# Optimization experiments

Hardware: AMD Instinct MI355X
Metric: run time of the kernel (lower is better)

Reference implementation:

```python
import jax, jax.numpy as jnp
import numpy as np

B, L, D_IN = 2, 4096, 512
H, D_K, D_V, D_OUT = 8, 64, 64, 512


def setup_inputs() -> dict:
    key = jax.random.key(0)
    k0, k1, k2, k3, k4 = jax.random.split(key, 5)
    x = jax.random.normal(k0, (B, L, D_IN), dtype=jnp.float32)
    W_q = jax.random.uniform(k1, (H, D_IN, D_K), dtype=jnp.float32)
    W_k = jax.random.uniform(k2, (H, D_IN, D_K), dtype=jnp.float32)
    W_v = jax.random.uniform(k3, (H, D_IN, D_V), dtype=jnp.float32)
    W_o = jax.random.uniform(k4, (H, D_V, D_OUT), dtype=jnp.float32)
    return {"x": x, "W_q": W_q, "W_k": W_k, "W_v": W_v, "W_o": W_o}


def reference(x, W_q, W_k, W_v, W_o):
    # x: (b, l, d_in); projections per head -> (b, h, l, d)
    Q = jnp.einsum('hjk,blj->bhlk', W_q, x)
    K = jnp.einsum('hjk,blj->bhlk', W_k, x)
    V = jnp.einsum('hjv,blj->bhlv', W_v, x)
    # no softmax: pure bilinear attention (Q K^T) V
    scores = jnp.einsum('bhik,bhjk->bhij', Q, K)          # (b, h, l, l)
    values = jnp.einsum('bhqk,bhkv->bhqv', scores, V)     # (b, h, l, d_v)
    return jnp.einsum('hvo,bhlv->blo', W_o, values)       # (b, l, d_out)
```

## Files before the change

### kernel.cpp

```cpp
#include <hip/hip_runtime.h>
#include <cstdint>


#define BDIM 2
#define LDIM 4096
#define DIN 512
#define HDIM 8
#define DK 64
#define DV 64
#define DOUT 512
#define NS 16

using bf16_t = __bf16;
typedef __bf16 bf16x8 __attribute__((ext_vector_type(8)));
typedef float floatx4 __attribute__((ext_vector_type(4)));

__device__ __forceinline__ unsigned short f2bf(float f) {
    unsigned int u = __builtin_bit_cast(unsigned int, f);
    u += 0x7FFFu + ((u >> 16) & 1u);
    return (unsigned short)(u >> 16);
}

__device__ __forceinline__ float bf2f(unsigned short s) {
    unsigned int u = ((unsigned int)s) << 16;
    return __builtin_bit_cast(float, u);
}

__device__ __forceinline__ void gld_lds16(const void* g, void* l) {
    __builtin_amdgcn_global_load_lds(
        (const __attribute__((address_space(1))) void*)g,
        (__attribute__((address_space(3))) void*)l, 16, 0, 0);
}

template <int BM, int BN, int BK, bool TRANS_OUT, int OUT_MODE>
__device__ __forceinline__ void gemm_core(const bf16_t* A, const bf16_t* B,
                                          void* Cp, int K, int lda, int ldb,
                                          int ldc, int tm, int tn) {
    constexpr int WM = BM / 2, WN = BN / 2;
    constexpr int FM = WM / 16, FN = WN / 16;
    constexpr int CPR = BK / 8;
    __shared__ bf16_t As[BM * BK];
    __shared__ bf16_t Bs[BN * BK];
    const int tid = threadIdx.x;
    const int lane = tid & 63;
    const int wr = (tid >> 7) & 1;
    const int wc = (tid >> 6) & 1;

    A += (size_t)tm * lda;
    B += (size_t)tn * ldb;

    floatx4 acc[FM][FN] = {};

    for (int k0 = 0; k0 < K; k0 += BK) {
#pragma unroll
        for (int i = 0; i < (BM * CPR) / 256; ++i) {
            int c = i * 256 + tid;
            int m = c / CPR, kc = c % CPR;
            gld_lds16(A + (size_t)m * lda + k0 + kc * 8, As + c * 8);
        }
#pragma unroll
        for (int i = 0; i < (BN * CPR) / 256; ++i) {
            int c = i * 256 + tid;
            int m = c / CPR, kc = c % CPR;
            gld_lds16(B + (size_t)m * ldb + k0 + kc * 8, Bs + c * 8);
        }
        __syncthreads();

#pragma unroll
        for (int kk = 0; kk < BK; kk += 32) {
            bf16x8 aF[FM], bF[FN];
#pragma unroll
            for (int fm = 0; fm < FM; ++fm)
                aF[fm] = *(const bf16x8*)(As + (wr * WM + fm * 16 + (lane & 15)) * BK +
                                          kk + (lane >> 4) * 8);
#pragma unroll
            for (int fn = 0; fn < FN; ++fn)
                bF[fn] = *(const bf16x8*)(Bs + (wc * WN + fn * 16 + (lane & 15)) * BK +
                                          kk + (lane >> 4) * 8);
#pragma unroll
            for (int fm = 0; fm < FM; ++fm)
#pragma unroll
                for (int fn = 0; fn < FN; ++fn)
                    acc[fm][fn] = __builtin_amdgcn_mfma_f32_16x16x32_bf16(
                        aF[fm], bF[fn], acc[fm][fn], 0, 0, 0);
        }
        __syncthreads();
    }

    const int cr4 = (lane >> 4) * 4;
    const int cn = lane & 15;
#pragma unroll
    for (int fm = 0; fm < FM; ++fm)
#pragma unroll
        for (int fn = 0; fn < FN; ++fn)
#pragma unroll
            for (int r = 0; r < 4; ++r) {
                int m = tm + wr * WM + fm * 16 + cr4 + r;
                int n = tn + wc * WN + fn * 16 + cn;
                size_t idx = TRANS_OUT ? ((size_t)n * ldc + m)
                                       : ((size_t)m * ldc + n);
                if (OUT_MODE == 0)
                    ((float*)Cp)[idx] = acc[fm][fn][r];
                else
                    ((unsigned short*)Cp)[idx] = f2bf(acc[fm][fn][r]);
            }
}

__global__ __launch_bounds__(256) void k_gram(const bf16_t* xT, unsigned short* Gp) {
    int z = blockIdx.z, b = z / NS, s = z % NS;
    const bf16_t* Ab = xT + (size_t)b * DIN * LDIM + s * (LDIM / NS);
    gemm_core<128, 128, 64, false, 1>(Ab, Ab, Gp + (size_t)z * DIN * DIN,
                                      LDIM / NS, LDIM, LDIM, DIN,
                                      blockIdx.x * 128, blockIdx.y * 128);
}

__global__ __launch_bounds__(256) void k_gred(const unsigned short* Gp,
                                              unsigned short* G16) {
    size_t gid = (size_t)blockIdx.x * 256 + threadIdx.x;
    int b = (int)(gid >> 15);
    size_t r = (gid & 32767) * 8;
    float s[8] = {};
#pragma unroll
    for (int sl = 0; sl < NS; ++sl) {
        const unsigned short* p = Gp + (((size_t)(b * NS + sl)) << 18) + r;
        uint4 v = *(const uint4*)p;
        unsigned int ws[4] = {v.x, v.y, v.z, v.w};
#pragma unroll
        for (int q = 0; q < 4; ++q) {
            s[q * 2 + 0] += bf2f((unsigned short)(ws[q] & 0xffffu));
            s[q * 2 + 1] += bf2f((unsigned short)(ws[q] >> 16));
        }
    }
    unsigned short o[8];
#pragma unroll
    for (int q = 0; q < 8; ++q) o[q] = f2bf(s[q]);
    *(uint4*)(G16 + (((size_t)b) << 18) + r) = *(const uint4*)o;
}

__global__ __launch_bounds__(256) void k_proj(const bf16_t* G16, const bf16_t* WvT,
                                              unsigned short* UT) {
    int b = blockIdx.z;
    gemm_core<64, 64, 32, true, 1>(G16 + (size_t)b * DIN * DIN, WvT,
                                   UT + (size_t)b * DIN * DIN, DIN, DIN, DIN,
                                   DIN, blockIdx.x * 64, blockIdx.y * 64);
}

__global__ __launch_bounds__(256) void k_m(const bf16_t* WkT, const bf16_t* UT,
                                           unsigned short* M) {
    int z = blockIdx.x, b = z >> 3, h = z & 7;
    gemm_core<64, 64, 32, false, 1>(WkT + (size_t)h * DK * DIN,
                                    UT + (size_t)b * DIN * DIN + (size_t)h * DV * DIN,
                                    M + (size_t)z * DK * DV, DIN, DIN, DIN, DV,
                                    0, 0);
}

__global__ __launch_bounds__(256) void k_tail(const bf16_t* WqC, const bf16_t* WoT,
                                              const bf16_t* M, unsigned short* CT) {
    int i0 = blockIdx.x * 64, o0 = blockIdx.y * 64, b = blockIdx.z;
    __shared__ bf16_t Aq[64 * 64];
    __shared__ bf16_t Ws[64 * 64];
    __shared__ bf16_t Msh[64 * 64];
    __shared__ bf16_t PTs[64 * 64];
    const int tid = threadIdx.x;
    const int lane = tid & 63;
    const int wr = (tid >> 7) & 1, wc = (tid >> 6) & 1;
    const int cr4 = (lane >> 4) * 4, cn = lane & 15;

    floatx4 acc[2][2] = {};

    for (int h = 0; h < HDIM; ++h) {
#pragma unroll
        for (int i = 0; i < 2; ++i) {
            int c = i * 256 + tid, m = c >> 3, kc = c & 7;
            gld_lds16(WqC + (size_t)(i0 + m) * DIN + h * 64 + kc * 8, Aq + c * 8);
            gld_lds16(WoT + ((size_t)h * DOUT + o0 + m) * DV + kc * 8, Ws + c * 8);
            gld_lds16(M + (((size_t)(b * HDIM + h)) << 12) + m * 64 + kc * 8,
                      Msh + c * 8);
        }
        __syncthreads();

        floatx4 pt[2][2] = {};
#pragma unroll
        for (int kk = 0; kk < 64; kk += 32) {
            bf16x8 aF[2], bF[2];
#pragma unroll
            for (int f = 0; f < 2; ++f) {
                aF[f] = *(const bf16x8*)(Ws + (wr * 32 + f * 16 + cn) * 64 + kk +
                                         (lane >> 4) * 8);
                bF[f] = *(const bf16x8*)(Msh + (wc * 32 + f * 16 + cn) * 64 + kk +
                                         (lane >> 4) * 8);
            }
#pragma unroll
            for (int fm = 0; fm < 2; ++fm)
#pragma unroll
                for (int fn = 0; fn < 2; ++fn)
                    pt[fm][fn] = __builtin_amdgcn_mfma_f32_16x16x32_bf16(
                        aF[fm], bF[fn], pt[fm][fn], 0, 0, 0);
        }
#pragma unroll
        for (int fm = 0; fm < 2; ++fm)
#pragma unroll
            for (int fn = 0; fn < 2; ++fn)
#pragma unroll
                for (int r = 0; r < 4; ++r) {
                    int m = wr * 32 + fm * 16 + cr4 + r;
                    int n = wc * 32 + fn * 16 + cn;
                    ((unsigned short*)PTs)[m * 64 + n] = f2bf(pt[fm][fn][r]);
                }
        __syncthreads();

#pragma unroll
        for (int kk = 0; kk < 64; kk += 32) {
            bf16x8 aF[2], bF[2];
#pragma unroll
            for (int f = 0; f < 2; ++f) {
                aF[f] = *(const bf16x8*)(PTs + (wr * 32 + f * 16 + cn) * 64 + kk +
                                         (lane >> 4) * 8);
                bF[f] = *(const bf16x8*)(Aq + (wc * 32 + f * 16 + cn) * 64 + kk +
                                         (lane >> 4) * 8);
            }
#pragma unroll
            for (int fm = 0; fm < 2; ++fm)
#pragma unroll
                for (int fn = 0; fn < 2; ++fn)
                    acc[fm][fn] = __builtin_amdgcn_mfma_f32_16x16x32_bf16(
                        aF[fm], bF[fn], acc[fm][fn], 0, 0, 0);
        }
        __syncthreads();
    }

    unsigned short* CTb = CT + (size_t)b * DIN * DOUT;
#pragma unroll
    for (int fm = 0; fm < 2; ++fm)
#pragma unroll
        for (int fn = 0; fn < 2; ++fn)
#pragma unroll
            for (int r = 0; r < 4; ++r) {
                int m = wr * 32 + fm * 16 + cr4 + r;
                int n = wc * 32 + fn * 16 + cn;
                CTb[(size_t)(o0 + m) * DIN + i0 + n] = f2bf(acc[fm][fn][r]);
            }
}

__global__ __launch_bounds__(256) void k_out(const bf16_t* x16, const bf16_t* CT,
                                             float* out) {
    int b = blockIdx.z;
    gemm_core<64, 128, 64, false, 0>(x16 + (size_t)b * LDIM * DIN,
                                     CT + (size_t)b * DIN * DOUT,
                                     out + (size_t)b * LDIM * DOUT, DIN, DIN,
                                     DIN, DOUT, blockIdx.x * 64,
                                     blockIdx.y * 128);
}

__global__ __launch_bounds__(256) void k_prep2(
    const float* x, const float* Wq, const float* Wk, const float* Wv,
    const float* Wo, unsigned short* xb, unsigned short* xT,
    unsigned short* WqC, unsigned short* WkT, unsigned short* WvT,
    unsigned short* WoT) {
    __shared__ unsigned short T[64][65];
    int tr = threadIdx.x >> 4, tc4 = (threadIdx.x & 15) * 4;
    int bid = blockIdx.x;
    if (bid < 1024) {
        int b = bid >> 9, r = bid & 511;
        int d0 = (r & 7) * 64, l0 = (r >> 3) * 64;
        const float* xp = x + (size_t)b * LDIM * DIN;
        unsigned short* xbp = xb + (size_t)b * LDIM * DIN;
#pragma unroll
        for (int p = 0; p < 4; ++p) {
            int l = p * 16 + tr;
            float4 v = *(const float4*)(xp + (size_t)(l0 + l) * DIN + d0 + tc4);
            unsigned short q0 = f2bf(v.x), q1 = f2bf(v.y), q2 = f2bf(v.z),
                           q3 = f2bf(v.w);
            *(ushort4*)(xbp + (size_t)(l0 + l) * DIN + d0 + tc4) =
                make_ushort4(q0, q1, q2, q3);
            T[l][tc4 + 0] = q0; T[l][tc4 + 1] = q1;
            T[l][tc4 + 2] = q2; T[l][tc4 + 3] = q3;
        }
        __syncthreads();
        unsigned short* xTp = xT + (size_t)b * DIN * LDIM;
#pragma unroll
        for (int p = 0; p < 4; ++p) {
            int d = p * 16 + tr;
            ushort4 u = make_ushort4(T[tc4 + 0][d], T[tc4 + 1][d], T[tc4 + 2][d],
                                     T[tc4 + 3][d]);
            *(ushort4*)(xTp + (size_t)(d0 + d) * LDIM + l0 + tc4) = u;
        }
        return;
    }
    int p_ = bid - 1024;
    int t = p_ & 7, job = (p_ >> 3) & 3, h = p_ >> 5;
    if (job == 0) {
        const float* src = Wq + (size_t)h * DIN * DK;
#pragma unroll
        for (int p = 0; p < 4; ++p) {
            int i = t * 64 + p * 16 + tr;
            float4 v = *(const float4*)(src + (size_t)i * DK + tc4);
            *(ushort4*)(WqC + (size_t)i * (HDIM * DK) + h * DK + tc4) =
                make_ushort4(f2bf(v.x), f2bf(v.y), f2bf(v.z), f2bf(v.w));
        }
        return;
    }
    const float* src;
    unsigned short* dst;
    int rows, cols, r0, c0;
    if (job == 1) {
        src = Wk + (size_t)h * DIN * DK; dst = WkT + (size_t)h * DK * DIN;
        rows = DIN; cols = DK; r0 = t * 64; c0 = 0;
    } else if (job == 2) {
        src = Wv + (size_t)h * DIN * DV; dst = WvT + (size_t)h * DV * DIN;
        rows = DIN; cols = DV; r0 = t * 64; c0 = 0;
    } else {
        src = Wo + (size_t)h * DV * DOUT; dst = WoT + (size_t)h * DOUT * DV;
        rows = DV; cols = DOUT; r0 = 0; c0 = t * 64;
    }
#pragma unroll
    for (int p = 0; p < 4; ++p) {
        int r = p * 16 + tr;
        float4 v = *(const float4*)(src + (size_t)(r0 + r) * cols + c0 + tc4);
        T[r][tc4 + 0] = f2bf(v.x); T[r][tc4 + 1] = f2bf(v.y);
        T[r][tc4 + 2] = f2bf(v.z); T[r][tc4 + 3] = f2bf(v.w);
    }
    __syncthreads();
#pragma unroll
    for (int p = 0; p < 4; ++p) {
        int c = p * 16 + tr;
        ushort4 u = make_ushort4(T[tc4 + 0][c], T[tc4 + 1][c], T[tc4 + 2][c],
                                 T[tc4 + 3][c]);
        *(ushort4*)(dst + (size_t)(c0 + c) * rows + r0 + tc4) = u;
    }
}

extern "C" void kernel_launch(void* const* d_in, const int* in_sizes, int n_in,
                              void* d_out, int out_size, void* d_ws, size_t ws_size,
                              hipStream_t stream) {
    const float* x  = (const float*)d_in[0];
    const float* Wq = (const float*)d_in[1];
    const float* Wk = (const float*)d_in[2];
    const float* Wv = (const float*)d_in[3];
    const float* Wo = (const float*)d_in[4];
    float* out = (float*)d_out;

    unsigned short* w = (unsigned short*)d_ws;
    unsigned short* xb16  = w; w += (size_t)BDIM * LDIM * DIN;
    unsigned short* xT16  = w; w += (size_t)BDIM * DIN * LDIM;
    unsigned short* WqC   = w; w += (size_t)DIN * HDIM * DK;
    unsigned short* WkT   = w; w += (size_t)HDIM * DK * DIN;
    unsigned short* WvT   = w; w += (size_t)HDIM * DV * DIN;
    unsigned short* WoT   = w; w += (size_t)HDIM * DOUT * DV;
    unsigned short* G16   = w; w += (size_t)BDIM * DIN * DIN;
    unsigned short* UT    = w; w += (size_t)BDIM * DIN * DIN;
    unsigned short* Mbuf  = w; w += (size_t)BDIM * HDIM * DK * DV;
    unsigned short* CT    = w; w += (size_t)BDIM * DIN * DOUT;
    unsigned short* Gp    = w; w += (size_t)BDIM * NS * DIN * DIN;

    k_prep2<<<dim3(1280), 256, 0, stream>>>(x, Wq, Wk, Wv, Wo, xb16, xT16,
                                            WqC, WkT, WvT, WoT);
    k_gram<<<dim3(4, 4, BDIM * NS), 256, 0, stream>>>((const bf16_t*)xT16, Gp);
    k_gred<<<dim3((BDIM * DIN * DIN) / (256 * 8)), 256, 0, stream>>>(Gp, G16);
    k_proj<<<dim3(8, 8, BDIM), 256, 0, stream>>>((const bf16_t*)G16,
                                                 (const bf16_t*)WvT, UT);
    k_m<<<dim3(BDIM * HDIM), 256, 0, stream>>>((const bf16_t*)WkT,
                                               (const bf16_t*)UT, Mbuf);
    k_tail<<<dim3(8, 8, BDIM), 256, 0, stream>>>((const bf16_t*)WqC,
                                                 (const bf16_t*)WoT,
                                                 (const bf16_t*)Mbuf, CT);
    k_out<<<dim3(LDIM / 64, DOUT / 128, BDIM), 256, 0, stream>>>(
        (const bf16_t*)xb16, (const bf16_t*)CT, out);
}
```

Before: 131.5 us.

## Fuse value projection and per-head M reduction into one kernel with atomics

Merges k_proj and k_m into a single kernel. Each block computes a 64-row slice of G·Wv for one head, keeps it in LDS, and immediately multiplies it by the matching Wk slice. Partial M products are summed into a float32 buffer with atomicAdd, which is zeroed by extra blocks added to the prep kernel. This drops one launch and the UT round trip through global memory, and replaces k_m's 16-block grid with a 128-block parallel reduction. The cost is atomic contention and float M reads with in-kernel conversion inside k_tail.

```diff
diff --git a/kernel.cpp b/kernel.cpp
--- a/kernel.cpp
+++ b/kernel.cpp
@@ -138,24 +138,90 @@
 }
 
 __global__ __launch_bounds__(256) void k_proj(const bf16_t* G16, const bf16_t* WvT,
-                                              unsigned short* UT) {
-    int b = blockIdx.z;
-    gemm_core<64, 64, 32, true, 1>(G16 + (size_t)b * DIN * DIN, WvT,
-                                   UT + (size_t)b * DIN * DIN, DIN, DIN, DIN,
-                                   DIN, blockIdx.x * 64, blockIdx.y * 64);
-}
-
-__global__ __launch_bounds__(256) void k_m(const bf16_t* WkT, const bf16_t* UT,
-                                           unsigned short* M) {
-    int z = blockIdx.x, b = z >> 3, h = z & 7;
-    gemm_core<64, 64, 32, false, 1>(WkT + (size_t)h * DK * DIN,
-                                    UT + (size_t)b * DIN * DIN + (size_t)h * DV * DIN,
-                                    M + (size_t)z * DK * DV, DIN, DIN, DIN, DV,
-                                    0, 0);
+                                              const bf16_t* WkT, float* M32) {
+    int i0 = blockIdx.x * 64, h = blockIdx.y, b = blockIdx.z;
+    __shared__ bf16_t As[64 * 32];
+    __shared__ bf16_t Bs[64 * 32];
+    __shared__ bf16_t Us[64 * 64];
+    __shared__ bf16_t Ks[64 * 64];
+    const int tid = threadIdx.x;
+    const int lane = tid & 63;
+    const int wr = (tid >> 7) & 1, wc = (tid >> 6) & 1;
+    const int cr4 = (lane >> 4) * 4, cn = lane & 15;
+
+    const bf16_t* A = G16 + (size_t)b * DIN * DIN + (size_t)i0 * DIN;
+    const bf16_t* B = WvT + (size_t)h * DV * DIN;
+    floatx4 acc[2][2] = {};
+    for (int k0 = 0; k0 < DIN; k0 += 32) {
+        int m = tid >> 2, kc = tid & 3;
+        gld_lds16(A + (size_t)m * DIN + k0 + kc * 8, As + tid * 8);
+        gld_lds16(B + (size_t)m * DIN + k0 + kc * 8, Bs + tid * 8);
+        __syncthreads();
+        bf16x8 aF[2], bF[2];
+#pragma unroll
+        for (int f = 0; f < 2; ++f) {
+            aF[f] = *(const bf16x8*)(As + (wr * 32 + f * 16 + cn) * 32 + (lane >> 4) * 8);
+            bF[f] = *(const bf16x8*)(Bs + (wc * 32 + f * 16 + cn) * 32 + (lane >> 4) * 8);
+        }
+#pragma unroll
+        for (int fm = 0; fm < 2; ++fm)
+#pragma unroll
+            for (int fn = 0; fn < 2; ++fn)
+                acc[fm][fn] = __builtin_amdgcn_mfma_f32_16x16x32_bf16(
+                    aF[fm], bF[fn], acc[fm][fn], 0, 0, 0);
+        __syncthreads();
+    }
+#pragma unroll
+    for (int fm = 0; fm < 2; ++fm)
+#pragma unroll
+        for (int fn = 0; fn < 2; ++fn)
+#pragma unroll
+            for (int r = 0; r < 4; ++r) {
+                int m = wr * 32 + fm * 16 + cr4 + r;
+                int n = wc * 32 + fn * 16 + cn;
+                ((unsigned short*)Us)[n * 64 + m] = f2bf(acc[fm][fn][r]);
+            }
+#pragma unroll
+    for (int i = 0; i < 2; ++i) {
+        int c = i * 256 + tid, m = c >> 3, kc = c & 7;
+        gld_lds16(WkT + (size_t)h * DK * DIN + (size_t)m * DIN + i0 + kc * 8,
+                  Ks + c * 8);
+    }
+    __syncthreads();
+
+    floatx4 mm[2][2] = {};
+#pragma unroll
+    for (int kk = 0; kk < 64; kk += 32) {
+        bf16x8 aF[2], bF[2];
+#pragma unroll
+        for (int f = 0; f < 2; ++f) {
+            aF[f] = *(const bf16x8*)(Ks + (wr * 32 + f * 16 + cn) * 64 + kk +
+                                     (lane >> 4) * 8);
+            bF[f] = *(const bf16x8*)(Us + (wc * 32 + f * 16 + cn) * 64 + kk +
+                                     (lane >> 4) * 8);
+        }
+#pragma unroll
+        for (int fm = 0; fm < 2; ++fm)
+#pragma unroll
+            for (int fn = 0; fn < 2; ++fn)
+                mm[fm][fn] = __builtin_amdgcn_mfma_f32_16x16x32_bf16(
+                    aF[fm], bF[fn], mm[fm][fn], 0, 0, 0);
+    }
+    float* Mh = M32 + ((size_t)(b * HDIM + h)) * (DK * DV);
+#pragma unroll
+    for (int fm = 0; fm < 2; ++fm)
+#pragma unroll
+        for (int fn = 0; fn < 2; ++fn)
+#pragma unroll
+            for (int r = 0; r < 4; ++r) {
+                int m = wr * 32 + fm * 16 + cr4 + r;
+                int n = wc * 32 + fn * 16 + cn;
+                atomicAdd(&Mh[m * 64 + n], mm[fm][fn][r]);
+            }
 }
 
 __global__ __launch_bounds__(256) void k_tail(const bf16_t* WqC, const bf16_t* WoT,
-                                              const bf16_t* M, unsigned short* CT) {
+                                              const float* M32, unsigned short* CT) {
     int i0 = blockIdx.x * 64, o0 = blockIdx.y * 64, b = blockIdx.z;
     __shared__ bf16_t Aq[64 * 64];
     __shared__ bf16_t Ws[64 * 64];
@@ -174,8 +240,14 @@
             int c = i * 256 + tid, m = c >> 3, kc = c & 7;
             gld_lds16(WqC + (size_t)(i0 + m) * DIN + h * 64 + kc * 8, Aq + c * 8);
             gld_lds16(WoT + ((size_t)h * DOUT + o0 + m) * DV + kc * 8, Ws + c * 8);
-            gld_lds16(M + (((size_t)(b * HDIM + h)) << 12) + m * 64 + kc * 8,
-                      Msh + c * 8);
+        }
+        const float* Mh = M32 + ((size_t)(b * HDIM + h)) * (DK * DV);
+#pragma unroll
+        for (int i = 0; i < 4; ++i) {
+            int idx = (i * 256 + tid) * 4;
+            float4 v = *(const float4*)(Mh + idx);
+            *(ushort4*)((unsigned short*)Msh + idx) =
+                make_ushort4(f2bf(v.x), f2bf(v.y), f2bf(v.z), f2bf(v.w));
         }
         __syncthreads();
 
@@ -256,10 +328,17 @@
     const float* x, const float* Wq, const float* Wk, const float* Wv,
     const float* Wo, unsigned short* xb, unsigned short* xT,
     unsigned short* WqC, unsigned short* WkT, unsigned short* WvT,
-    unsigned short* WoT) {
+    unsigned short* WoT, float* M32) {
     __shared__ unsigned short T[64][65];
     int tr = threadIdx.x >> 4, tc4 = (threadIdx.x & 15) * 4;
     int bid = blockIdx.x;
+    if (bid >= 1280) {
+        size_t g = ((size_t)(bid - 1280) * 256 + threadIdx.x) * 32;
+        float4 z4 = make_float4(0.f, 0.f, 0.f, 0.f);
+#pragma unroll
+        for (int q = 0; q < 8; ++q) *(float4*)(M32 + g + q * 4) = z4;
+        return;
+    }
     if (bid < 1024) {
         int b = bid >> 9, r = bid & 511;
         int d0 = (r & 7) * 64, l0 = (r >> 3) * 64;
@@ -348,22 +427,19 @@
     unsigned short* WvT   = w; w += (size_t)HDIM * DV * DIN;
     unsigned short* WoT   = w; w += (size_t)HDIM * DOUT * DV;
     unsigned short* G16   = w; w += (size_t)BDIM * DIN * DIN;
-    unsigned short* UT    = w; w += (size_t)BDIM * DIN * DIN;
-    unsigned short* Mbuf  = w; w += (size_t)BDIM * HDIM * DK * DV;
     unsigned short* CT    = w; w += (size_t)BDIM * DIN * DOUT;
     unsigned short* Gp    = w; w += (size_t)BDIM * NS * DIN * DIN;
-
-    k_prep2<<<dim3(1280), 256, 0, stream>>>(x, Wq, Wk, Wv, Wo, xb16, xT16,
-                                            WqC, WkT, WvT, WoT);
+    float* M32 = (float*)(((uintptr_t)w + 255) & ~(uintptr_t)255);
+
+    k_prep2<<<dim3(1288), 256, 0, stream>>>(x, Wq, Wk, Wv, Wo, xb16, xT16,
+                                            WqC, WkT, WvT, WoT, M32);
     k_gram<<<dim3(4, 4, BDIM * NS), 256, 0, stream>>>((const bf16_t*)xT16, Gp);
     k_gred<<<dim3((BDIM * DIN * DIN) / (256 * 8)), 256, 0, stream>>>(Gp, G16);
     k_proj<<<dim3(8, 8, BDIM), 256, 0, stream>>>((const bf16_t*)G16,
-                                                 (const bf16_t*)WvT, UT);
-    k_m<<<dim3(BDIM * HDIM), 256, 0, stream>>>((const bf16_t*)WkT,
-                                               (const bf16_t*)UT, Mbuf);
+                                                 (const bf16_t*)WvT,
+                                                 (const bf16_t*)WkT, M32);
     k_tail<<<dim3(8, 8, BDIM), 256, 0, stream>>>((const bf16_t*)WqC,
-                                                 (const bf16_t*)WoT,
-                                                 (const bf16_t*)Mbuf, CT);
+                                                 (const bf16_t*)WoT, M32, CT);
     k_out<<<dim3(LDIM / 64, DOUT / 128, BDIM), 256, 0, stream>>>(
         (const bf16_t*)xb16, (const bf16_t*)CT, out);
 }
```

After: 128.5 us. 1.02x faster.

## Replace Gram-matrix path with direct K/V projection and split-K atomic M

Applied to the files above, without the earlier changes.

Drops the x^T x Gram matrix route (gram, split reduction, projection and M kernels). Instead it computes K and V for all heads in one GEMM against concatenated transposed weights, then forms M = K^T V per head with a split-L GEMM that accumulates through float atomics into a buffer zeroed in the prep kernel. This removes the transposed copy of x and the bf16 partial-sum reduction, and cuts the launch count. In exchange it performs more FLOPs at the projection step, writes a larger KVT intermediate, and relies on atomics.

```diff
diff --git a/kernel.cpp b/kernel.cpp
--- a/kernel.cpp
+++ b/kernel.cpp
@@ -9,7 +9,7 @@
 #define DK 64
 #define DV 64
 #define DOUT 512
-#define NS 16
+#define MSPLIT 8
 
 using bf16_t = __bf16;
 typedef __bf16 bf16x8 __attribute__((ext_vector_type(8)));
@@ -19,11 +19,6 @@
     unsigned int u = __builtin_bit_cast(unsigned int, f);
     u += 0x7FFFu + ((u >> 16) & 1u);
     return (unsigned short)(u >> 16);
-}
-
-__device__ __forceinline__ float bf2f(unsigned short s) {
-    unsigned int u = ((unsigned int)s) << 16;
-    return __builtin_bit_cast(float, u);
 }
 
 __device__ __forceinline__ void gld_lds16(const void* g, void* l) {
@@ -101,61 +96,33 @@
                                        : ((size_t)m * ldc + n);
                 if (OUT_MODE == 0)
                     ((float*)Cp)[idx] = acc[fm][fn][r];
+                else if (OUT_MODE == 1)
+                    ((unsigned short*)Cp)[idx] = f2bf(acc[fm][fn][r]);
                 else
-                    ((unsigned short*)Cp)[idx] = f2bf(acc[fm][fn][r]);
+                    atomicAdd(&((float*)Cp)[idx], acc[fm][fn][r]);
             }
 }
 
-__global__ __launch_bounds__(256) void k_gram(const bf16_t* xT, unsigned short* Gp) {
-    int z = blockIdx.z, b = z / NS, s = z % NS;
-    const bf16_t* Ab = xT + (size_t)b * DIN * LDIM + s * (LDIM / NS);
-    gemm_core<128, 128, 64, false, 1>(Ab, Ab, Gp + (size_t)z * DIN * DIN,
-                                      LDIM / NS, LDIM, LDIM, DIN,
-                                      blockIdx.x * 128, blockIdx.y * 128);
-}
-
-__global__ __launch_bounds__(256) void k_gred(const unsigned short* Gp,
-                                              unsigned short* G16) {
-    size_t gid = (size_t)blockIdx.x * 256 + threadIdx.x;
-    int b = (int)(gid >> 15);
-    size_t r = (gid & 32767) * 8;
-    float s[8] = {};
-#pragma unroll
-    for (int sl = 0; sl < NS; ++sl) {
-        const unsigned short* p = Gp + (((size_t)(b * NS + sl)) << 18) + r;
-        uint4 v = *(const uint4*)p;
-        unsigned int ws[4] = {v.x, v.y, v.z, v.w};
-#pragma unroll
-        for (int q = 0; q < 4; ++q) {
-            s[q * 2 + 0] += bf2f((unsigned short)(ws[q] & 0xffffu));
-            s[q * 2 + 1] += bf2f((unsigned short)(ws[q] >> 16));
-        }
-    }
-    unsigned short o[8];
-#pragma unroll
-    for (int q = 0; q < 8; ++q) o[q] = f2bf(s[q]);
-    *(uint4*)(G16 + (((size_t)b) << 18) + r) = *(const uint4*)o;
-}
-
-__global__ __launch_bounds__(256) void k_proj(const bf16_t* G16, const bf16_t* WvT,
-                                              unsigned short* UT) {
+__global__ __launch_bounds__(256) void k_kv(const bf16_t* xb16, const bf16_t* WkvT,
+                                            unsigned short* KVT) {
     int b = blockIdx.z;
-    gemm_core<64, 64, 32, true, 1>(G16 + (size_t)b * DIN * DIN, WvT,
-                                   UT + (size_t)b * DIN * DIN, DIN, DIN, DIN,
-                                   DIN, blockIdx.x * 64, blockIdx.y * 64);
-}
-
-__global__ __launch_bounds__(256) void k_m(const bf16_t* WkT, const bf16_t* UT,
-                                           unsigned short* M) {
-    int z = blockIdx.x, b = z >> 3, h = z & 7;
-    gemm_core<64, 64, 32, false, 1>(WkT + (size_t)h * DK * DIN,
-                                    UT + (size_t)b * DIN * DIN + (size_t)h * DV * DIN,
-                                    M + (size_t)z * DK * DV, DIN, DIN, DIN, DV,
-                                    0, 0);
+    gemm_core<128, 128, 64, true, 1>(xb16 + (size_t)b * LDIM * DIN, WkvT,
+                                     KVT + (size_t)b * 1024 * LDIM, DIN, DIN,
+                                     DIN, LDIM, blockIdx.x * 128,
+                                     blockIdx.y * 128);
+}
+
+__global__ __launch_bounds__(256) void k_msplit(const bf16_t* KVT, float* M32) {
+    int s = blockIdx.x, z = blockIdx.y, b = z >> 3, h = z & 7;
+    const bf16_t* base = KVT + (size_t)b * 1024 * LDIM + s * (LDIM / MSPLIT);
+    const bf16_t* A = base + (size_t)(h * 64) * LDIM;
+    const bf16_t* B = base + (size_t)(512 + h * 64) * LDIM;
+    gemm_core<64, 64, 64, false, 2>(A, B, M32 + (size_t)z * DK * DV,
+                                    LDIM / MSPLIT, LDIM, LDIM, DV, 0, 0);
 }
 
 __global__ __launch_bounds__(256) void k_tail(const bf16_t* WqC, const bf16_t* WoT,
-                                              const bf16_t* M, unsigned short* CT) {
+                                              const float* M32, unsigned short* CT) {
     int i0 = blockIdx.x * 64, o0 = blockIdx.y * 64, b = blockIdx.z;
     __shared__ bf16_t Aq[64 * 64];
     __shared__ bf16_t Ws[64 * 64];
@@ -174,8 +141,14 @@
             int c = i * 256 + tid, m = c >> 3, kc = c & 7;
             gld_lds16(WqC + (size_t)(i0 + m) * DIN + h * 64 + kc * 8, Aq + c * 8);
             gld_lds16(WoT + ((size_t)h * DOUT + o0 + m) * DV + kc * 8, Ws + c * 8);
-            gld_lds16(M + (((size_t)(b * HDIM + h)) << 12) + m * 64 + kc * 8,
-                      Msh + c * 8);
+        }
+        const float* Mh = M32 + ((size_t)(b * HDIM + h)) * (DK * DV);
+#pragma unroll
+        for (int i = 0; i < 4; ++i) {
+            int idx = (i * 256 + tid) * 4;
+            float4 v = *(const float4*)(Mh + idx);
+            *(ushort4*)((unsigned short*)Msh + idx) =
+                make_ushort4(f2bf(v.x), f2bf(v.y), f2bf(v.z), f2bf(v.w));
         }
         __syncthreads();
 
@@ -254,40 +227,28 @@
 
 __global__ __launch_bounds__(256) void k_prep2(
     const float* x, const float* Wq, const float* Wk, const float* Wv,
-    const float* Wo, unsigned short* xb, unsigned short* xT,
-    unsigned short* WqC, unsigned short* WkT, unsigned short* WvT,
-    unsigned short* WoT) {
+    const float* Wo, unsigned short* xb, unsigned short* WqC,
+    unsigned short* WkvT, unsigned short* WoT, float* M32) {
     __shared__ unsigned short T[64][65];
     int tr = threadIdx.x >> 4, tc4 = (threadIdx.x & 15) * 4;
     int bid = blockIdx.x;
-    if (bid < 1024) {
-        int b = bid >> 9, r = bid & 511;
-        int d0 = (r & 7) * 64, l0 = (r >> 3) * 64;
-        const float* xp = x + (size_t)b * LDIM * DIN;
-        unsigned short* xbp = xb + (size_t)b * LDIM * DIN;
-#pragma unroll
-        for (int p = 0; p < 4; ++p) {
-            int l = p * 16 + tr;
-            float4 v = *(const float4*)(xp + (size_t)(l0 + l) * DIN + d0 + tc4);
-            unsigned short q0 = f2bf(v.x), q1 = f2bf(v.y), q2 = f2bf(v.z),
-                           q3 = f2bf(v.w);
-            *(ushort4*)(xbp + (size_t)(l0 + l) * DIN + d0 + tc4) =
-                make_ushort4(q0, q1, q2, q3);
-            T[l][tc4 + 0] = q0; T[l][tc4 + 1] = q1;
-            T[l][tc4 + 2] = q2; T[l][tc4 + 3] = q3;
-        }
-        __syncthreads();
-        unsigned short* xTp = xT + (size_t)b * DIN * LDIM;
-#pragma unroll
-        for (int p = 0; p < 4; ++p) {
-            int d = p * 16 + tr;
-            ushort4 u = make_ushort4(T[tc4 + 0][d], T[tc4 + 1][d], T[tc4 + 2][d],
-                                     T[tc4 + 3][d]);
-            *(ushort4*)(xTp + (size_t)(d0 + d) * LDIM + l0 + tc4) = u;
-        }
+    if (bid < 2048) {
+        size_t base = ((size_t)bid * 256 + threadIdx.x) * 8;
+        float4 v0 = *(const float4*)(x + base);
+        float4 v1 = *(const float4*)(x + base + 4);
+        unsigned short o[8] = {f2bf(v0.x), f2bf(v0.y), f2bf(v0.z), f2bf(v0.w),
+                               f2bf(v1.x), f2bf(v1.y), f2bf(v1.z), f2bf(v1.w)};
+        *(uint4*)(xb + base) = *(const uint4*)o;
         return;
     }
-    int p_ = bid - 1024;
+    if (bid >= 2304) {
+        size_t g = ((size_t)(bid - 2304) * 256 + threadIdx.x) * 32;
+        float4 z4 = make_float4(0.f, 0.f, 0.f, 0.f);
+#pragma unroll
+        for (int q = 0; q < 8; ++q) *(float4*)(M32 + g + q * 4) = z4;
+        return;
+    }
+    int p_ = bid - 2048;
     int t = p_ & 7, job = (p_ >> 3) & 3, h = p_ >> 5;
     if (job == 0) {
         const float* src = Wq + (size_t)h * DIN * DK;
@@ -304,10 +265,10 @@
     unsigned short* dst;
     int rows, cols, r0, c0;
     if (job == 1) {
-        src = Wk + (size_t)h * DIN * DK; dst = WkT + (size_t)h * DK * DIN;
+        src = Wk + (size_t)h * DIN * DK; dst = WkvT + (size_t)(h * 64) * DIN;
         rows = DIN; cols = DK; r0 = t * 64; c0 = 0;
     } else if (job == 2) {
-        src = Wv + (size_t)h * DIN * DV; dst = WvT + (size_t)h * DV * DIN;
+        src = Wv + (size_t)h * DIN * DV; dst = WkvT + (size_t)(512 + h * 64) * DIN;
         rows = DIN; cols = DV; r0 = t * 64; c0 = 0;
     } else {
         src = Wo + (size_t)h * DV * DOUT; dst = WoT + (size_t)h * DOUT * DV;
@@ -342,28 +303,21 @@
 
     unsigned short* w = (unsigned short*)d_ws;
     unsigned short* xb16  = w; w += (size_t)BDIM * LDIM * DIN;
-    unsigned short* xT16  = w; w += (size_t)BDIM * DIN * LDIM;
     unsigned short* WqC   = w; w += (size_t)DIN * HDIM * DK;
-    unsigned short* WkT   = w; w += (size_t)HDIM * DK * DIN;
-    unsigned short* WvT   = w; w += (size_t)HDIM * DV * DIN;
+    unsigned short* WkvT  = w; w += (size_t)1024 * DIN;
     unsigned short* WoT   = w; w += (size_t)HDIM * DOUT * DV;
-    unsigned short* G16   = w; w += (size_t)BDIM * DIN * DIN;
-    unsigned short* UT    = w; w += (size_t)BDIM * DIN * DIN;
-    unsigned short* Mbuf  = w; w += (size_t)BDIM * HDIM * DK * DV;
+    unsigned short* KVT   = w; w += (size_t)BDIM * 1024 * LDIM;
     unsigned short* CT    = w; w += (size_t)BDIM * DIN * DOUT;
-    unsigned short* Gp    = w; w += (size_t)BDIM * NS * DIN * DIN;
-
-    k_prep2<<<dim3(1280), 256, 0, stream>>>(x, Wq, Wk, Wv, Wo, xb16, xT16,
-                                            WqC, WkT, WvT, WoT);
-    k_gram<<<dim3(4, 4, BDIM * NS), 256, 0, stream>>>((const bf16_t*)xT16, Gp);
-    k_gred<<<dim3((BDIM * DIN * DIN) / (256 * 8)), 256, 0, stream>>>(Gp, G16);
-    k_proj<<<dim3(8, 8, BDIM), 256, 0, stream>>>((const bf16_t*)G16,
-                                                 (const bf16_t*)WvT, UT);
-    k_m<<<dim3(BDIM * HDIM), 256, 0, stream>>>((const bf16_t*)WkT,
-                                               (const bf16_t*)UT, Mbuf);
+    float* M32 = (float*)(((uintptr_t)w + 255) & ~(uintptr_t)255);
+
+    k_prep2<<<dim3(2312), 256, 0, stream>>>(x, Wq, Wk, Wv, Wo, xb16, WqC,
+                                            WkvT, WoT, M32);
+    k_kv<<<dim3(32, 8, BDIM), 256, 0, stream>>>((const bf16_t*)xb16,
+                                                (const bf16_t*)WkvT, KVT);
+    k_msplit<<<dim3(MSPLIT, BDIM * HDIM), 256, 0, stream>>>((const bf16_t*)KVT,
+                                                            M32);
     k_tail<<<dim3(8, 8, BDIM), 256, 0, stream>>>((const bf16_t*)WqC,
-                                                 (const bf16_t*)WoT,
-                                                 (const bf16_t*)Mbuf, CT);
+                                                 (const bf16_t*)WoT, M32, CT);
     k_out<<<dim3(LDIM / 64, DOUT / 128, BDIM), 256, 0, stream>>>(
         (const bf16_t*)xb16, (const bf16_t*)CT, out);
 }
```

Measured after the change: 128.2 us. 2.5% less time.
